# Kernel optimization log

Measured on AMD Instinct MI355X. Metric: run time of the kernel, lower is better.

## Reference

```python
import jax, jax.numpy as jnp
import numpy as np

IMG_H, IMG_W = 512.0, 512.0
PRED_SIZES = [(64, 64), (32, 32), (16, 16), (8, 8), (4, 4), (2, 2)]
ASPECT_RATIOS = [1.0, 2.0, 0.5, 3.0]
SCALES = [0.04, 0.1, 0.26, 0.42, 0.58, 0.74]
N_CLASSES = 21
CONF_THRESH = 0.01
IOU_THRESH = 0.45
TOP_K = 100
NMS_MAX = 200
XY_VAR, WH_VAR = 0.1, 0.2
NEG = -1e30  # stand-in for -inf that is safe under autodiff


def generate_boxes():
    # Standard SSD anchors (cx, cy, w, h), normalized to [0, 1].
    all_boxes = []
    for (fh, fw), s in zip(PRED_SIZES, SCALES):
        cx = (np.arange(fw, dtype=np.float32) + 0.5) / fw
        cy = (np.arange(fh, dtype=np.float32) + 0.5) / fh
        cxg, cyg = np.meshgrid(cx, cy)  # [fh, fw]
        for ar in ASPECT_RATIOS:
            w = s * np.sqrt(ar)
            h = s / np.sqrt(ar)
            b = np.stack([cxg, cyg, np.full_like(cxg, w), np.full_like(cxg, h)], axis=-1)
            all_boxes.append(b.reshape(-1, 4))
    return np.concatenate(all_boxes, axis=0).astype(np.float32)  # [21840, 4]


def setup_inputs() -> dict:
    key = jax.random.key(0)
    n_boxes = sum(fh * fw for fh, fw in PRED_SIZES) * len(ASPECT_RATIOS)
    y_pred = jax.random.normal(key, (32, n_boxes, N_CLASSES + 4), dtype=jnp.float32)
    box_tensor = jnp.asarray(generate_boxes())
    return {"y_pred": y_pred, "box_tensor": box_tensor}


def _decode(y_pred, box_tensor):
    # y_pred: [B, N, C+4], box_tensor: [N, 4] (cx, cy, w, h)
    logits = y_pred[..., :-4]
    class_ids = jnp.argmax(logits, axis=-1).astype(jnp.float32)  # [B, N]
    confidences = jnp.max(logits, axis=-1)                       # [B, N]
    a_cx, a_cy, a_w, a_h = box_tensor[:, 0], box_tensor[:, 1], box_tensor[:, 2], box_tensor[:, 3]
    cx = y_pred[..., -4] * XY_VAR * a_w + a_cx
    cy = y_pred[..., -3] * XY_VAR * a_h + a_cy
    w = jnp.exp(y_pred[..., -2] * WH_VAR) * a_w
    h = jnp.exp(y_pred[..., -1] * WH_VAR) * a_h
    xmin = jnp.clip(cx - 0.5 * w, 0.0, 1.0)
    ymin = jnp.clip(cy - 0.5 * h, 0.0, 1.0)
    xmax = jnp.clip(cx + 0.5 * w, 0.0, 1.0)
    ymax = jnp.clip(cy + 0.5 * h, 0.0, 1.0)
    # [B, N, 6]: class_id, confidence, xmin, ymin, xmax, ymax
    return jnp.stack([class_ids, confidences, xmin, ymin, xmax, ymax], axis=-1)


def _nms_image(preds):
    # preds: [N, 6]. Greedy NMS over confident, non-background boxes, then top-k.
    N = preds.shape[0]
    valid = (preds[:, 0] != 0.0) & (preds[:, 1] > CONF_THRESH)
    scores0 = jnp.where(valid, preds[:, 1], NEG)
    boxes = preds[:, 2:6]  # xmin, ymin, xmax, ymax
    areas = (boxes[:, 2] - boxes[:, 0]) * (boxes[:, 3] - boxes[:, 1])
    idxs = jnp.arange(N)

    def step(scores, _):
        i = jnp.argmax(scores)
        best = scores[i]
        ok = best > NEG * 0.5
        b = boxes[i]
        ix1 = jnp.maximum(b[0], boxes[:, 0])
        iy1 = jnp.maximum(b[1], boxes[:, 1])
        ix2 = jnp.minimum(b[2], boxes[:, 2])
        iy2 = jnp.minimum(b[3], boxes[:, 3])
        inter = jnp.maximum(ix2 - ix1, 0.0) * jnp.maximum(iy2 - iy1, 0.0)
        union = areas[i] + areas - inter
        iou = jnp.where(union > 0.0, inter / jnp.maximum(union, 1e-12), 0.0)
        suppress = (iou > IOU_THRESH) | (idxs == i)
        new_scores = jnp.where(ok & suppress, NEG, scores)
        row = jnp.where(ok, preds[i], 0.0)         # zero-pad like the TF pad path
        s = jnp.where(ok, best, 0.0)               # pad rows get score 0
        return new_scores, (row, s)

    _, (rows, sel_scores) = jax.lax.scan(step, scores0, None, length=NMS_MAX)
    # rows: [NMS_MAX, 6] in descending score order; top_k like the TF layer.
    _, ti = jax.lax.top_k(sel_scores, TOP_K)
    return rows[ti]  # [TOP_K, 6]


def reference(y_pred, box_tensor):
    preds = _decode(y_pred, box_tensor)          # [B, N, 6]
    return jax.vmap(_nms_image)(preds)           # [B, TOP_K, 6]
```

## Files before the change

### kernel.cpp

```cpp
#include <hip/hip_runtime.h>
#include <math.h>

typedef unsigned long long ull;
typedef unsigned int uint;

#define NBOX 21840
#define SEGSZ 512
#define NSEG 44
#define NPAD (NSEG*SEGSZ)
#define PFXS 46
#define OUTW 47
#define NWALK (NSEG*PFXS)
#define MCAP 2048
#define BATCH 32
#define NCLS 21
#define NEGV -1e30f
#define MIOU (15099494.5/33554432.0)

__device__ __forceinline__ uint key_hi(float s) {
    uint b = __float_as_uint(s);
    uint m = (uint)((int)b >> 31) | 0x80000000u;
    return ~(b ^ m);
}
__device__ __forceinline__ float key_score(uint hi) {
    uint srt = ~hi;
    uint b = (srt & 0x80000000u) ? (srt ^ 0x80000000u) : ~srt;
    return __uint_as_float(b);
}

__device__ __forceinline__ float area_of(float4 b) {
    return __fmul_rn(__fsub_rn(b.z, b.x), __fsub_rn(b.w, b.y));
}
__device__ __forceinline__ bool sup_check(float4 a, float aarea, float4 c, float carea) {
    float ix1 = fmaxf(a.x, c.x), iy1 = fmaxf(a.y, c.y);
    float ix2 = fminf(a.z, c.z), iy2 = fminf(a.w, c.w);
    float inter = __fmul_rn(fmaxf(__fsub_rn(ix2, ix1), 0.f), fmaxf(__fsub_rn(iy2, iy1), 0.f));
    float uni = __fsub_rn(__fadd_rn(aarea, carea), inter);
    return (uni > 0.f) && ((double)inter > MIOU * (double)fmaxf(uni, 1e-12f));
}

__device__ __forceinline__ ull cex_shfl(ull v, int j, bool asc, int lane) {
    ull pv = __shfl_xor(v, j);
    bool keepmin = (((lane & j) == 0) == asc);
    bool less = (v < pv);
    return (keepmin == less) ? v : pv;
}

__global__ __launch_bounds__(512) void decode_sort_kernel(
    const float* __restrict__ y_pred, const float* __restrict__ box_tensor,
    float4* __restrict__ BX, ull* __restrict__ KS, ull* __restrict__ KS2)
{
    __shared__ float st[SEGSZ * 25];
    __shared__ ull sk[SEGSZ];
    int img = blockIdx.y, seg = blockIdx.x, tid = threadIdx.x;
    int b0 = seg * SEGSZ;
    int nval = NBOX - b0; nval = nval < 0 ? 0 : (nval > SEGSZ ? SEGSZ : nval);
    if (nval > 0) {
        const float* src = y_pred + ((size_t)img * NBOX + b0) * 25;
        int nf = nval * 25, nf4 = nf >> 2;
        const float4* src4 = (const float4*)src;
        float4* st4 = (float4*)st;
        for (int f = tid; f < nf4; f += 512) st4[f] = src4[f];
        for (int f = (nf4 << 2) + tid; f < nf; f += 512) st[f] = src[f];
    }
    __syncthreads();
    int i = b0 + tid;
    size_t o = (size_t)img * NPAD + i;
    ull v;
    if (tid < nval) {
        const float* yl = st + tid * 25;
        float best = yl[0]; int bi = 0;
        #pragma unroll
        for (int k = 1; k < NCLS; k++) { float x = yl[k]; if (x > best) { best = x; bi = k; } }
        float4 a = ((const float4*)box_tensor)[i];
        float t0 = yl[21], t1 = yl[22], t2 = yl[23], t3 = yl[24];
        float cx = __fadd_rn(__fmul_rn(__fmul_rn(t0, 0.1f), a.z), a.x);
        float cy = __fadd_rn(__fmul_rn(__fmul_rn(t1, 0.1f), a.w), a.y);
        float w  = __fmul_rn((float)exp((double)__fmul_rn(t2, 0.2f)), a.z);
        float h  = __fmul_rn((float)exp((double)__fmul_rn(t3, 0.2f)), a.w);
        float hw = __fmul_rn(0.5f, w), hh = __fmul_rn(0.5f, h);
        float xmin = fminf(fmaxf(__fsub_rn(cx, hw), 0.f), 1.f);
        float ymin = fminf(fmaxf(__fsub_rn(cy, hh), 0.f), 1.f);
        float xmax = fminf(fmaxf(__fadd_rn(cx, hw), 0.f), 1.f);
        float ymax = fminf(fmaxf(__fadd_rn(cy, hh), 0.f), 1.f);
        bool valid = (bi != 0) && (best > 0.01f);
        BX[o] = make_float4(xmin, ymin, xmax, ymax);
        uint hi = valid ? key_hi(best) : __float_as_uint(NEGV);
        v = ((ull)hi << 32) | ((uint)(i << 8)) | (uint)bi;
    } else {
        v = ((ull)__float_as_uint(NEGV) << 32) | ((uint)(i << 8));
    }
    int lane = tid & 63;
    for (int k = 2; k <= SEGSZ; k <<= 1) {
        for (int j = k >> 1; j >= 64; j >>= 1) {
            sk[tid] = v; __syncthreads();
            ull pv = sk[tid ^ j];
            bool keepmin = (((tid & j) == 0) == ((tid & k) == 0));
            bool less = (v < pv);
            v = (keepmin == less) ? v : pv;
            __syncthreads();
        }
        int j0 = (k >> 1) < 32 ? (k >> 1) : 32;
        for (int j = j0; j >= 1; j >>= 1)
            v = cex_shfl(v, j, (tid & k) == 0, lane);
    }
    KS[(size_t)img * NPAD + b0 + tid] = v;
    if (tid < OUTW) KS2[(size_t)img * (NSEG * OUTW) + seg * OUTW + tid] = v;
}

__global__ __launch_bounds__(512) void nms_kernel(
    const ull* __restrict__ KS2, const ull* __restrict__ KS,
    const float4* __restrict__ BX, float* __restrict__ out)
{
    __shared__ ull klist[MCAP];
    __shared__ ull pref[NSEG];
    __shared__ float4 accbox[100];
    __shared__ float  accarea[100];

    int img = blockIdx.x, tid = threadIdx.x;
    int wid = tid >> 6, lane = tid & 63;
    const ull* ks2i = KS2 + (size_t)img * (NSEG * OUTW);

    ull v[4];
    #pragma unroll
    for (int r = 0; r < 4; r++) {
        int e = (wid << 8) + (r << 6) + lane;
        v[r] = (e < NWALK) ? ks2i[(e / PFXS) * OUTW + (e % PFXS)] : ~0ull;
    }
    if (tid < NSEG) pref[tid] = ks2i[tid * OUTW + PFXS];

    for (int k = 2; k <= MCAP; k <<= 1) {
        int jl = k >> 1;
        if (jl >= 64) {
            #pragma unroll
            for (int r = 0; r < 4; r++) klist[(wid << 8) + (r << 6) + lane] = v[r];
            for (int j = jl; j >= 64; j >>= 1) {
                __syncthreads();
                for (int t = tid; t < MCAP / 2; t += 512) {
                    int i = ((t & ~(j - 1)) << 1) | (t & (j - 1));
                    int l = i | j;
                    ull a = klist[i], b = klist[l];
                    if ((a > b) == ((i & k) == 0)) { klist[i] = b; klist[l] = a; }
                }
            }
            __syncthreads();
            #pragma unroll
            for (int r = 0; r < 4; r++) v[r] = klist[(wid << 8) + (r << 6) + lane];
        }
        int j0 = jl < 32 ? jl : 32;
        for (int j = j0; j >= 1; j >>= 1) {
            #pragma unroll
            for (int r = 0; r < 4; r++) {
                int e = (wid << 8) + (r << 6) + lane;
                v[r] = cex_shfl(v[r], j, (e & k) == 0, lane);
            }
        }
    }
    #pragma unroll
    for (int r = 0; r < 4; r++) klist[(wid << 8) + (r << 6) + lane] = v[r];
    __syncthreads();

    if (tid >= 64) return;
    const float4* BXg = BX + (size_t)img * NPAD;
    const ull*    ksg = KS + (size_t)img * NPAD;
    float* orow = out + (size_t)img * 600;

    ull cutk = ~0ull;
    for (int s = 0; s < NSEG; s++) { ull x = pref[s]; if (x < cutk) cutk = x; }

    int A = 0, stop = 0, done = 0;

    ull pk = klist[lane];
    float4 pbox = make_float4(0.f, 0.f, 0.f, 0.f);
    if (!(pk >> 63)) pbox = BXg[((uint)pk) >> 8];

    for (int base = 0; base < MCAP && !stop; base += 64) {
        ull kk = pk; float4 bb = pbox;
        {
            int c = base + 64 + lane;
            pk = (c < MCAP) ? klist[c] : ~0ull;
            pbox = make_float4(0.f, 0.f, 0.f, 0.f);
            if (!(pk >> 63)) pbox = BXg[((uint)pk) >> 8];
        }
        bool valid = !(kk >> 63) && (kk < cutk);
        ull vmask = __ballot(valid);
        float carea = area_of(bb);

        bool p = false;
        for (int a = 0; a < A; a++)
            p = p || sup_check(accbox[a], accarea[a], bb, carea);

        ull cand = __ballot(valid && !p);
        while (cand && A < 100) {
            int i = __ffsll((ull)cand) - 1;
            float4 ib = make_float4(__shfl(bb.x, i), __shfl(bb.y, i),
                                    __shfl(bb.z, i), __shfl(bb.w, i));
            float ia = __shfl(carea, i);
            ull row = __ballot(sup_check(ib, ia, bb, carea));
            if (lane == i) {
                accbox[A] = bb; accarea[A] = carea;
                uint hi = (uint)(kk >> 32), lo = (uint)kk;
                orow[A * 6 + 0] = (float)(lo & 0xffu);
                orow[A * 6 + 1] = key_score(hi);
                orow[A * 6 + 2] = bb.x; orow[A * 6 + 3] = bb.y;
                orow[A * 6 + 4] = bb.z; orow[A * 6 + 5] = bb.w;
            }
            A++;
            cand &= ~(1ull << i);
            cand &= ~row;
        }
        if (A >= 100) { stop = 1; done = 1; }
        else if (vmask != ~0ull) {
            stop = 1;
            int fi = __ffsll((ull)~vmask) - 1;
            ull fk = __shfl(kk, fi);
            done = (fk >= cutk) ? (int)(cutk >> 63) : 1;
        }
        __builtin_amdgcn_wave_barrier();
    }
    if (!stop) done = (int)(cutk >> 63);

    if (!done && A < 100) {
        ull nextk = cutk;
        while (A < 100) {
            ull best = ~0ull;
            for (int e = lane; e < NPAD; e += 64) {
                ull kk2 = ksg[e];
                if (kk2 >= nextk && kk2 < best) best = kk2;
            }
            #pragma unroll
            for (int off = 32; off; off >>= 1) {
                ull oo = __shfl_xor(best, off);
                if (oo < best) best = oo;
            }
            if (best >> 63) break;
            uint bhi = (uint)(best >> 32), blo = (uint)best;
            float4 cb = BXg[blo >> 8];
            float ca = area_of(cb);
            bool sup2 = false;
            #pragma unroll
            for (int t = 0; t < 2; t++) {
                int slot = lane + 64 * t;
                if (slot < A && sup_check(accbox[slot], accarea[slot], cb, ca)) sup2 = true;
            }
            if (__ballot(sup2) == 0ull) {
                if (lane == 0) {
                    accbox[A] = cb; accarea[A] = ca;
                    orow[A * 6 + 0] = (float)(blo & 0xffu);
                    orow[A * 6 + 1] = key_score(bhi);
                    orow[A * 6 + 2] = cb.x; orow[A * 6 + 3] = cb.y;
                    orow[A * 6 + 4] = cb.z; orow[A * 6 + 5] = cb.w;
                }
                A++;
            }
            nextk = best + 1;
            __builtin_amdgcn_wave_barrier();
        }
    }

    for (int r = lane; r < (100 - A) * 6; r += 64) orow[A * 6 + r] = 0.f;
}

extern "C" void kernel_launch(void* const* d_in, const int* in_sizes, int n_in,
                              void* d_out, int out_size, void* d_ws, size_t ws_size,
                              hipStream_t stream)
{
    const float* y_pred     = (const float*)d_in[0];
    const float* box_tensor = (const float*)d_in[1];
    float* out = (float*)d_out;

    size_t stride = (size_t)BATCH * NPAD;
    ull*    KS  = (ull*)d_ws;
    float4* BX  = (float4*)(KS + stride);
    ull*    KS2 = (ull*)(BX + stride);

    decode_sort_kernel<<<dim3(NSEG, BATCH), 512, 0, stream>>>(y_pred, box_tensor, BX, KS, KS2);
    nms_kernel<<<BATCH, 512, 0, stream>>>(KS2, KS, BX, out);
}
```

Before: 154.9 us.

## Precompute pairwise IoU suppression bitmask matrix for top 512 candidates across block

All 512 threads now build a 512x512 suppression bitmask matrix (IoU > threshold) over the first 512 sorted candidates in shared memory. A single wave then runs greedy NMS by OR-ing bit rows, with no serial IoU checks. Candidates beyond 512 still go through the old wave-level scan and the fallback global search. This spreads the serial single-wave IoU work across the whole block, at the cost of computing the full matrix even when few boxes get selected.

```diff
diff --git a/kernel.cpp b/kernel.cpp
--- a/kernel.cpp
+++ b/kernel.cpp
@@ -12,6 +12,7 @@
 #define OUTW 47
 #define NWALK (NSEG*PFXS)
 #define MCAP 2048
+#define MTX 512
 #define BATCH 32
 #define NCLS 21
 #define NEGV -1e30f
@@ -113,13 +114,18 @@
     const float4* __restrict__ BX, float* __restrict__ out)
 {
     __shared__ ull klist[MCAP];
+    __shared__ ull rows[MTX][8];
+    __shared__ float4 cbox[MTX];
+    __shared__ float4 accbox[100];
     __shared__ ull pref[NSEG];
-    __shared__ float4 accbox[100];
-    __shared__ float  accarea[100];
+    __shared__ int limsh;
 
     int img = blockIdx.x, tid = threadIdx.x;
     int wid = tid >> 6, lane = tid & 63;
     const ull* ks2i = KS2 + (size_t)img * (NSEG * OUTW);
+    const float4* BXg = BX + (size_t)img * NPAD;
+
+    if (tid == 0) limsh = 0;
 
     ull v[4];
     #pragma unroll
@@ -158,103 +164,169 @@
     }
     #pragma unroll
     for (int r = 0; r < 4; r++) klist[(wid << 8) + (r << 6) + lane] = v[r];
-    __syncthreads();
-
-    if (tid >= 64) return;
-    const float4* BXg = BX + (size_t)img * NPAD;
-    const ull*    ksg = KS + (size_t)img * NPAD;
-    float* orow = out + (size_t)img * 600;
 
     ull cutk = ~0ull;
     for (int s = 0; s < NSEG; s++) { ull x = pref[s]; if (x < cutk) cutk = x; }
-
-    int A = 0, stop = 0, done = 0;
-
-    ull pk = klist[lane];
-    float4 pbox = make_float4(0.f, 0.f, 0.f, 0.f);
-    if (!(pk >> 63)) pbox = BXg[((uint)pk) >> 8];
-
-    for (int base = 0; base < MCAP && !stop; base += 64) {
-        ull kk = pk; float4 bb = pbox;
-        {
-            int c = base + 64 + lane;
-            pk = (c < MCAP) ? klist[c] : ~0ull;
-            pbox = make_float4(0.f, 0.f, 0.f, 0.f);
-            if (!(pk >> 63)) pbox = BXg[((uint)pk) >> 8];
-        }
-        bool valid = !(kk >> 63) && (kk < cutk);
-        ull vmask = __ballot(valid);
-        float carea = area_of(bb);
-
-        bool p = false;
-        for (int a = 0; a < A; a++)
-            p = p || sup_check(accbox[a], accarea[a], bb, carea);
-
-        ull cand = __ballot(valid && !p);
-        while (cand && A < 100) {
-            int i = __ffsll((ull)cand) - 1;
-            float4 ib = make_float4(__shfl(bb.x, i), __shfl(bb.y, i),
-                                    __shfl(bb.z, i), __shfl(bb.w, i));
-            float ia = __shfl(carea, i);
-            ull row = __ballot(sup_check(ib, ia, bb, carea));
-            if (lane == i) {
-                accbox[A] = bb; accarea[A] = carea;
-                uint hi = (uint)(kk >> 32), lo = (uint)kk;
-                orow[A * 6 + 0] = (float)(lo & 0xffu);
-                orow[A * 6 + 1] = key_score(hi);
-                orow[A * 6 + 2] = bb.x; orow[A * 6 + 3] = bb.y;
-                orow[A * 6 + 4] = bb.z; orow[A * 6 + 5] = bb.w;
-            }
-            A++;
-            cand &= ~(1ull << i);
-            cand &= ~row;
-        }
-        if (A >= 100) { stop = 1; done = 1; }
-        else if (vmask != ~0ull) {
-            stop = 1;
-            int fi = __ffsll((ull)~vmask) - 1;
-            ull fk = __shfl(kk, fi);
-            done = (fk >= cutk) ? (int)(cutk >> 63) : 1;
-        }
-        __builtin_amdgcn_wave_barrier();
-    }
-    if (!stop) done = (int)(cutk >> 63);
-
-    if (!done && A < 100) {
-        ull nextk = cutk;
-        while (A < 100) {
-            ull best = ~0ull;
-            for (int e = lane; e < NPAD; e += 64) {
-                ull kk2 = ksg[e];
-                if (kk2 >= nextk && kk2 < best) best = kk2;
-            }
-            #pragma unroll
-            for (int off = 32; off; off >>= 1) {
-                ull oo = __shfl_xor(best, off);
-                if (oo < best) best = oo;
-            }
-            if (best >> 63) break;
-            uint bhi = (uint)(best >> 32), blo = (uint)best;
-            float4 cb = BXg[blo >> 8];
-            float ca = area_of(cb);
-            bool sup2 = false;
-            #pragma unroll
-            for (int t = 0; t < 2; t++) {
-                int slot = lane + 64 * t;
-                if (slot < A && sup_check(accbox[slot], accarea[slot], cb, ca)) sup2 = true;
-            }
-            if (__ballot(sup2) == 0ull) {
-                if (lane == 0) {
-                    accbox[A] = cb; accarea[A] = ca;
-                    orow[A * 6 + 0] = (float)(blo & 0xffu);
-                    orow[A * 6 + 1] = key_score(bhi);
-                    orow[A * 6 + 2] = cb.x; orow[A * 6 + 3] = cb.y;
-                    orow[A * 6 + 4] = cb.z; orow[A * 6 + 5] = cb.w;
-                }
-                A++;
-            }
-            nextk = best + 1;
-            __builtin_amdgcn_wave_barrier();
+    ull limk = (cutk < (1ull << 63)) ? cutk : (1ull << 63);
+    int cnt = 0;
+    #pragma unroll
+    for (int r = 0; r < 4; r++) cnt += __popcll(__ballot(v[r] < limk));
+    if (lane == 0) atomicAdd(&limsh, cnt);
+    __syncthreads();
+    int lim = limsh;
+
+    {
+        ull k = klist[tid];
+        cbox[tid] = (k >> 63) ? make_float4(9.f, 9.f, 9.f, 9.f) : BXg[((uint)k) >> 8];
+    }
+    __syncthreads();
+
+    for (int r = wid; r < MTX; r += 8) {
+        float4 rb = cbox[r];
+        float ra = area_of(rb);
+        int w0 = r >> 6;
+        ull myword = 0;
+        #pragma unroll
+        for (int wi = 0; wi < 8; wi++) {
+            ull m = 0;
+            if (wi >= w0) {
+                int j = (wi << 6) + lane;
+                float4 jb = cbox[j];
+                bool s = (j > r) && sup_check(rb, ra, jb, area_of(jb));
+                m = __ballot(s);
+            }
+            if (lane == wi) myword = m;
+        }
+        if (lane < 8) rows[r][lane] = myword;
+    }
+    __syncthreads();
+
+    if (tid >= 64) return;
+    float* orow = out + (size_t)img * 600;
+    const ull* ksg = KS + (size_t)img * NPAD;
+
+    ull S[8];
+    #pragma unroll
+    for (int w = 0; w < 8; w++) S[w] = 0;
+    int lim512 = lim < MTX ? lim : MTX;
+    int A = 0;
+    int acc0 = 0, acc1 = 0;
+
+    for (;;) {
+        int c = MTX;
+        #pragma unroll
+        for (int w = 7; w >= 0; w--) {
+            ull m = ~S[w];
+            if (m) c = (w << 6) + __ffsll(m) - 1;
+        }
+        if (c >= lim512) break;
+        #pragma unroll
+        for (int w = 0; w < 8; w++) {
+            ull rr = rows[c][w];
+            if (w == (c >> 6)) rr |= 1ull << (c & 63);
+            S[w] |= rr;
+        }
+        if (lane == (A & 63)) { if (A < 64) acc0 = c; else acc1 = c; }
+        A++;
+        if (A >= 100) break;
+    }
+    int accA = A;
+
+    if (lane < accA) {
+        int c = acc0; ull k = klist[c]; float4 b = cbox[c];
+        float* o = orow + lane * 6;
+        o[0] = (float)((uint)k & 0xffu); o[1] = key_score((uint)(k >> 32));
+        o[2] = b.x; o[3] = b.y; o[4] = b.z; o[5] = b.w;
+    }
+    if (64 + lane < accA) {
+        int c = acc1; ull k = klist[c]; float4 b = cbox[c];
+        float* o = orow + (64 + lane) * 6;
+        o[0] = (float)((uint)k & 0xffu); o[1] = key_score((uint)(k >> 32));
+        o[2] = b.x; o[3] = b.y; o[4] = b.z; o[5] = b.w;
+    }
+
+    int done = 1;
+    if (A < 100) {
+        if (lane < A)      accbox[lane]      = cbox[acc0];
+        if (64 + lane < A) accbox[64 + lane] = cbox[acc1];
+        done = 0;
+        if (lim <= MTX) {
+            done = (int)(cutk >> 63);
+        } else {
+            int stop = 0;
+            for (int base = MTX; base < MCAP && !stop; base += 64) {
+                int pos = base + lane;
+                ull kk = klist[pos];
+                bool valid = pos < lim;
+                ull vmask = __ballot(valid);
+                float4 bb = (kk >> 63) ? make_float4(9.f,9.f,9.f,9.f) : BXg[((uint)kk) >> 8];
+                float ca = area_of(bb);
+                bool pr = false;
+                for (int a = 0; a < A; a++) {
+                    float4 ab = accbox[a];
+                    pr = pr || sup_check(ab, area_of(ab), bb, ca);
+                }
+                ull cand = __ballot(valid && !pr);
+                while (cand && A < 100) {
+                    int i = __ffsll(cand) - 1;
+                    float4 ib = make_float4(__shfl(bb.x, i), __shfl(bb.y, i),
+                                            __shfl(bb.z, i), __shfl(bb.w, i));
+                    float ia = __shfl(ca, i);
+                    ull row = __ballot(sup_check(ib, ia, bb, ca));
+                    if (lane == i) {
+                        accbox[A] = bb;
+                        float* o = orow + A * 6;
+                        o[0] = (float)((uint)kk & 0xffu); o[1] = key_score((uint)(kk >> 32));
+                        o[2] = bb.x; o[3] = bb.y; o[4] = bb.z; o[5] = bb.w;
+                    }
+                    A++;
+                    cand &= ~(1ull << i);
+                    cand &= ~row;
+                }
+                if (A >= 100) { stop = 1; done = 1; }
+                else if (vmask != ~0ull) { stop = 1; done = (int)(cutk >> 63); }
+                __builtin_amdgcn_wave_barrier();
+            }
+            if (!stop) done = (int)(cutk >> 63);
+        }
+        if (!done && A < 100) {
+            ull nextk = cutk;
+            while (A < 100) {
+                ull best = ~0ull;
+                for (int e = lane; e < NPAD; e += 64) {
+                    ull kk2 = ksg[e];
+                    if (kk2 >= nextk && kk2 < best) best = kk2;
+                }
+                #pragma unroll
+                for (int off = 32; off; off >>= 1) {
+                    ull oo = __shfl_xor(best, off);
+                    if (oo < best) best = oo;
+                }
+                if (best >> 63) break;
+                uint bhi = (uint)(best >> 32), blo = (uint)best;
+                float4 cb = BXg[blo >> 8];
+                float ca2 = area_of(cb);
+                bool sup2 = false;
+                #pragma unroll
+                for (int t = 0; t < 2; t++) {
+                    int slot = lane + 64 * t;
+                    if (slot < A) {
+                        float4 ab = accbox[slot];
+                        if (sup_check(ab, area_of(ab), cb, ca2)) sup2 = true;
+                    }
+                }
+                if (__ballot(sup2) == 0ull) {
+                    if (lane == 0) {
+                        accbox[A] = cb;
+                        float* o = orow + A * 6;
+                        o[0] = (float)(blo & 0xffu); o[1] = key_score(bhi);
+                        o[2] = cb.x; o[3] = cb.y; o[4] = cb.z; o[5] = cb.w;
+                    }
+                    A++;
+                }
+                nextk = best + 1;
+                __builtin_amdgcn_wave_barrier();
+            }
         }
     }
 
```

New measurement: 217.0 us. +40.1%, slower.

## Precompute intra-chunk suppression bitmasks in parallel and cut bitonic sort syncs

Applied to the files above, without the earlier changes.

After sorting, all 8 waves work together to fetch boxes for the first 1024 candidates into shared memory and build a per-candidate 64-bit mask of which earlier boxes in the same 64-chunk suppress it. The serial single-wave greedy walk then reads this mask instead of doing a shuffle plus ballot IoU check for each accepted box, and defers output writes to one batched store. The bitonic sort also handles strides 64 and 128 inside registers, which removes two block-wide barrier stages per merge level. The cost is extra shared memory and mask computation for candidates the walk may never reach.

```diff
diff --git a/kernel.cpp b/kernel.cpp
--- a/kernel.cpp
+++ b/kernel.cpp
@@ -12,6 +12,7 @@
 #define OUTW 47
 #define NWALK (NSEG*PFXS)
 #define MCAP 2048
+#define WIN 1024
 #define BATCH 32
 #define NCLS 21
 #define NEGV -1e30f
@@ -113,13 +114,16 @@
     const float4* __restrict__ BX, float* __restrict__ out)
 {
     __shared__ ull klist[MCAP];
-    __shared__ ull pref[NSEG];
+    __shared__ float4 cbox[WIN];
+    __shared__ ull scol[WIN];
     __shared__ float4 accbox[100];
     __shared__ float  accarea[100];
+    __shared__ ull pref[NSEG];
 
     int img = blockIdx.x, tid = threadIdx.x;
     int wid = tid >> 6, lane = tid & 63;
     const ull* ks2i = KS2 + (size_t)img * (NSEG * OUTW);
+    const float4* BXg = BX + (size_t)img * NPAD;
 
     ull v[4];
     #pragma unroll
@@ -130,13 +134,14 @@
     if (tid < NSEG) pref[tid] = ks2i[tid * OUTW + PFXS];
 
     for (int k = 2; k <= MCAP; k <<= 1) {
-        int jl = k >> 1;
-        if (jl >= 64) {
+        if ((k >> 1) >= 256) {
             #pragma unroll
             for (int r = 0; r < 4; r++) klist[(wid << 8) + (r << 6) + lane] = v[r];
-            for (int j = jl; j >= 64; j >>= 1) {
+            for (int j = k >> 1; j >= 256; j >>= 1) {
                 __syncthreads();
-                for (int t = tid; t < MCAP / 2; t += 512) {
+                #pragma unroll
+                for (int h = 0; h < 2; h++) {
+                    int t = tid + (h << 9);
                     int i = ((t & ~(j - 1)) << 1) | (t & (j - 1));
                     int l = i | j;
                     ull a = klist[i], b = klist[l];
@@ -147,7 +152,23 @@
             #pragma unroll
             for (int r = 0; r < 4; r++) v[r] = klist[(wid << 8) + (r << 6) + lane];
         }
-        int j0 = jl < 32 ? jl : 32;
+        #pragma unroll
+        for (int jr = 2; jr >= 1; jr >>= 1) {
+            int j = jr << 6;
+            if ((k >> 1) >= j) {
+                #pragma unroll
+                for (int r = 0; r < 4; r++) {
+                    if ((r & jr) == 0) {
+                        int rh = r | jr;
+                        int e = (wid << 8) + (r << 6) + lane;
+                        bool asc = ((e & k) == 0);
+                        ull a = v[r], b = v[rh];
+                        if ((a > b) == asc) { v[r] = b; v[rh] = a; }
+                    }
+                }
+            }
+        }
+        int j0 = (k >> 1) < 32 ? (k >> 1) : 32;
         for (int j = j0; j >= 1; j >>= 1) {
             #pragma unroll
             for (int r = 0; r < 4; r++) {
@@ -160,65 +181,116 @@
     for (int r = 0; r < 4; r++) klist[(wid << 8) + (r << 6) + lane] = v[r];
     __syncthreads();
 
+    for (int b = wid; b < (WIN >> 6); b += 8) {
+        int c = (b << 6) + lane;
+        ull k = klist[c];
+        float4 bx = BXg[((uint)k) >> 8];
+        cbox[c] = bx;
+        float myar = area_of(bx);
+        ull col = 0;
+        #pragma unroll 4
+        for (int i = 0; i < 64; i++) {
+            float4 ib = cbox[(b << 6) + i];
+            bool s = (i < lane) && sup_check(ib, area_of(ib), bx, myar);
+            col |= ((ull)s) << i;
+        }
+        scol[c] = col;
+    }
+    __syncthreads();
+
     if (tid >= 64) return;
-    const float4* BXg = BX + (size_t)img * NPAD;
-    const ull*    ksg = KS + (size_t)img * NPAD;
     float* orow = out + (size_t)img * 600;
+    const ull* ksg = KS + (size_t)img * NPAD;
 
     ull cutk = ~0ull;
     for (int s = 0; s < NSEG; s++) { ull x = pref[s]; if (x < cutk) cutk = x; }
 
     int A = 0, stop = 0, done = 0;
-
-    ull pk = klist[lane];
-    float4 pbox = make_float4(0.f, 0.f, 0.f, 0.f);
-    if (!(pk >> 63)) pbox = BXg[((uint)pk) >> 8];
-
-    for (int base = 0; base < MCAP && !stop; base += 64) {
-        ull kk = pk; float4 bb = pbox;
-        {
-            int c = base + 64 + lane;
-            pk = (c < MCAP) ? klist[c] : ~0ull;
-            pbox = make_float4(0.f, 0.f, 0.f, 0.f);
-            if (!(pk >> 63)) pbox = BXg[((uint)pk) >> 8];
-        }
+    int acc0 = 0, acc1 = 0;
+
+    for (int base = 0; base < WIN && !stop; base += 64) {
+        int c = base + lane;
+        ull kk = klist[c];
+        float4 bb = cbox[c];
+        float ca = area_of(bb);
+        ull mycol = scol[c];
         bool valid = !(kk >> 63) && (kk < cutk);
         ull vmask = __ballot(valid);
-        float carea = area_of(bb);
-
-        bool p = false;
+        bool alive = valid;
         for (int a = 0; a < A; a++)
-            p = p || sup_check(accbox[a], accarea[a], bb, carea);
-
-        ull cand = __ballot(valid && !p);
-        while (cand && A < 100) {
-            int i = __ffsll((ull)cand) - 1;
-            float4 ib = make_float4(__shfl(bb.x, i), __shfl(bb.y, i),
-                                    __shfl(bb.z, i), __shfl(bb.w, i));
-            float ia = __shfl(carea, i);
-            ull row = __ballot(sup_check(ib, ia, bb, carea));
-            if (lane == i) {
-                accbox[A] = bb; accarea[A] = carea;
-                uint hi = (uint)(kk >> 32), lo = (uint)kk;
-                orow[A * 6 + 0] = (float)(lo & 0xffu);
-                orow[A * 6 + 1] = key_score(hi);
-                orow[A * 6 + 2] = bb.x; orow[A * 6 + 3] = bb.y;
-                orow[A * 6 + 4] = bb.z; orow[A * 6 + 5] = bb.w;
-            }
+            alive = alive && !sup_check(accbox[a], accarea[a], bb, ca);
+        ull m = __ballot(alive);
+        while (m && A < 100) {
+            int i = __ffsll(m) - 1;
+            if (lane == i) { accbox[A] = bb; accarea[A] = ca; }
+            if (lane == (A & 63)) { if (A < 64) acc0 = base + i; else acc1 = base + i; }
             A++;
-            cand &= ~(1ull << i);
-            cand &= ~row;
+            m &= ~(1ull << i);
+            m &= __ballot(!((mycol >> i) & 1ull));
         }
         if (A >= 100) { stop = 1; done = 1; }
         else if (vmask != ~0ull) {
             stop = 1;
-            int fi = __ffsll((ull)~vmask) - 1;
+            int fi = __ffsll(~vmask) - 1;
             ull fk = __shfl(kk, fi);
             done = (fk >= cutk) ? (int)(cutk >> 63) : 1;
         }
         __builtin_amdgcn_wave_barrier();
     }
-    if (!stop) done = (int)(cutk >> 63);
+
+    int accW = A;
+    if (lane < accW) {
+        ull k = klist[acc0]; float4 b = cbox[acc0];
+        float* o = orow + lane * 6;
+        o[0] = (float)((uint)k & 0xffu); o[1] = key_score((uint)(k >> 32));
+        o[2] = b.x; o[3] = b.y; o[4] = b.z; o[5] = b.w;
+    }
+    if (64 + lane < accW) {
+        ull k = klist[acc1]; float4 b = cbox[acc1];
+        float* o = orow + (64 + lane) * 6;
+        o[0] = (float)((uint)k & 0xffu); o[1] = key_score((uint)(k >> 32));
+        o[2] = b.x; o[3] = b.y; o[4] = b.z; o[5] = b.w;
+    }
+
+    if (!stop) {
+        for (int base = WIN; base < MCAP && !stop; base += 64) {
+            int pos = base + lane;
+            ull kk = klist[pos];
+            bool valid = !(kk >> 63) && (kk < cutk);
+            ull vmask = __ballot(valid);
+            float4 bb = BXg[((uint)kk) >> 8];
+            float ca = area_of(bb);
+            bool alive = valid;
+            for (int a = 0; a < A; a++)
+                alive = alive && !sup_check(accbox[a], accarea[a], bb, ca);
+            ull cand = __ballot(alive);
+            while (cand && A < 100) {
+                int i = __ffsll(cand) - 1;
+                float4 ib = make_float4(__shfl(bb.x, i), __shfl(bb.y, i),
+                                        __shfl(bb.z, i), __shfl(bb.w, i));
+                float ia = __shfl(ca, i);
+                ull row = __ballot(sup_check(ib, ia, bb, ca));
+                if (lane == i) {
+                    accbox[A] = bb; accarea[A] = ca;
+                    float* o = orow + A * 6;
+                    o[0] = (float)((uint)kk & 0xffu); o[1] = key_score((uint)(kk >> 32));
+                    o[2] = bb.x; o[3] = bb.y; o[4] = bb.z; o[5] = bb.w;
+                }
+                A++;
+                cand &= ~(1ull << i);
+                cand &= ~row;
+            }
+            if (A >= 100) { stop = 1; done = 1; }
+            else if (vmask != ~0ull) {
+                stop = 1;
+                int fi = __ffsll(~vmask) - 1;
+                ull fk = __shfl(kk, fi);
+                done = (fk >= cutk) ? (int)(cutk >> 63) : 1;
+            }
+            __builtin_amdgcn_wave_barrier();
+        }
+        if (!stop) done = (int)(cutk >> 63);
+    }
 
     if (!done && A < 100) {
         ull nextk = cutk;
@@ -236,20 +308,19 @@
             if (best >> 63) break;
             uint bhi = (uint)(best >> 32), blo = (uint)best;
             float4 cb = BXg[blo >> 8];
-            float ca = area_of(cb);
+            float ca2 = area_of(cb);
             bool sup2 = false;
             #pragma unroll
             for (int t = 0; t < 2; t++) {
                 int slot = lane + 64 * t;
-                if (slot < A && sup_check(accbox[slot], accarea[slot], cb, ca)) sup2 = true;
+                if (slot < A && sup_check(accbox[slot], accarea[slot], cb, ca2)) sup2 = true;
             }
             if (__ballot(sup2) == 0ull) {
                 if (lane == 0) {
-                    accbox[A] = cb; accarea[A] = ca;
-                    orow[A * 6 + 0] = (float)(blo & 0xffu);
-                    orow[A * 6 + 1] = key_score(bhi);
-                    orow[A * 6 + 2] = cb.x; orow[A * 6 + 3] = cb.y;
-                    orow[A * 6 + 4] = cb.z; orow[A * 6 + 5] = cb.w;
+                    accbox[A] = cb; accarea[A] = ca2;
+                    float* o = orow + A * 6;
+                    o[0] = (float)(blo & 0xffu); o[1] = key_score(bhi);
+                    o[2] = cb.x; o[3] = cb.y; o[4] = cb.z; o[5] = cb.w;
                 }
                 A++;
             }
```

Result: slower. 161.0 us (+3.9%).
